# Optimization experiments

Hardware: AMD Instinct MI355X
Metric: run time of the kernel (lower is better)

Reference implementation:

```python
import jax
import jax.numpy as jnp
import numpy as np

SAMPLE_RATE = 22050
CUTOFF = 0.4 * SAMPLE_RATE  # 0.8 * (sample_rate * 0.5)
Q = 0.707  # torchaudio default


def _biquad_coeffs():
    # torchaudio.functional.lowpass_biquad coefficient formulas
    w0 = 2.0 * np.pi * CUTOFF / SAMPLE_RATE  # = 0.8*pi
    alpha = np.sin(w0) / (2.0 * Q)
    cosw = np.cos(w0)
    a0 = 1.0 + alpha
    b0 = (1.0 - cosw) / 2.0 / a0
    b1 = (1.0 - cosw) / a0
    b2 = b0
    a1 = -2.0 * cosw / a0
    a2 = (1.0 - alpha) / a0
    return np.float32(b0), np.float32(b1), np.float32(b2), np.float32(a1), np.float32(a2)


def setup_inputs() -> dict:
    key = jax.random.key(0)
    inputs = jax.random.normal(key, (64, 262144), dtype=jnp.float32)
    return {"inputs": inputs}


def reference(inputs):
    b0, b1, b2, a1, a2 = _biquad_coeffs()
    x = inputs  # [B, T]
    # FIR (numerator) part, fully parallel
    x1 = jnp.pad(x[:, :-1], ((0, 0), (1, 0)))
    x2 = jnp.pad(x[:, :-2], ((0, 0), (2, 0)))
    u = b0 * x + b1 * x1 + b2 * x2  # [B, T]

    # IIR (denominator) recurrence: y[t] = u[t] - a1*y[t-1] - a2*y[t-2]
    def step(carry, ut):
        y1, y2 = carry
        y = ut - a1 * y1 - a2 * y2
        return (y, y1), y

    z = jnp.zeros(x.shape[0], dtype=x.dtype)
    _, ys = jax.lax.scan(step, (z, z), u.T)  # scan over time, carry [B]
    # torchaudio lfilter clamps output to [-1, 1] by default
    return jnp.clip(ys.T, -1.0, 1.0)
```

## Files before the change

### kernel.cpp

```cpp
#include <hip/hip_runtime.h>
#include <math.h>

constexpr int T_LEN = 262144;
constexpr int CH    = 16;
constexpr int WARM  = 24;
constexpr int TPB   = 256;
constexpr int SEG   = TPB * CH;
constexpr int BPR   = T_LEN / SEG;
constexpr int NLD   = (CH + WARM) / 4;

__device__ __forceinline__ int sw(int i) { return i ^ (((i >> 4) & 7) << 2); }

__global__ __launch_bounds__(TPB, 6) void lowpass_kernel(
    const float* __restrict__ x, float* __restrict__ out,
    float b0, float b1, float b2, float a1, float a2)
{
    __shared__ float lds[SEG];
    const int tid = threadIdx.x;
    const size_t rbase = (size_t)(blockIdx.x / BPR) * T_LEN;
    const int seg0 = (blockIdx.x % BPR) * SEG;
    const float* __restrict__ xr = x   + rbase;
    float*       __restrict__ yr = out + rbase;

    const int w0 = seg0 + 16 * tid - WARM;
    float4 xv[NLD];
    #pragma unroll
    for (int j = 0; j < NLD; ++j) {
        const int gp = w0 + 4 * j;
        xv[j] = (gp >= 0) ? *reinterpret_cast<const float4*>(xr + gp)
                          : make_float4(0.f, 0.f, 0.f, 0.f);
    }

    float x1 = 0.f, x2 = 0.f, y1 = 0.f, y2 = 0.f;
    auto step = [&](float xc) -> float {
        const float u = fmaf(b0, xc, fmaf(b1, x1, b2 * x2));
        const float y = fmaf(-a1, y1, fmaf(-a2, y2, u));
        x2 = x1; x1 = xc; y2 = y1; y1 = y;
        return y;
    };

    #pragma unroll
    for (int j = 0; j < WARM / 4; ++j) {
        step(xv[j].x); step(xv[j].y); step(xv[j].z); step(xv[j].w);
    }
    float4 ov[CH / 4];
    #pragma unroll
    for (int k = 0; k < CH / 4; ++k) {
        const float4 v = xv[WARM / 4 + k];
        ov[k].x = fminf(fmaxf(step(v.x), -1.f), 1.f);
        ov[k].y = fminf(fmaxf(step(v.y), -1.f), 1.f);
        ov[k].z = fminf(fmaxf(step(v.z), -1.f), 1.f);
        ov[k].w = fminf(fmaxf(step(v.w), -1.f), 1.f);
    }

    #pragma unroll
    for (int k = 0; k < CH / 4; ++k)
        *reinterpret_cast<float4*>(&lds[sw(16 * tid + 4 * k)]) = ov[k];
    __syncthreads();

    #pragma unroll
    for (int j = 0; j < SEG / 4 / TPB; ++j) {
        const int m = tid + j * TPB;
        const float4 v = *reinterpret_cast<const float4*>(&lds[sw(4 * m)]);
        *reinterpret_cast<float4*>(yr + seg0 + 4 * m) = v;
    }
}

extern "C" void kernel_launch(void* const* d_in, const int* in_sizes, int n_in,
                              void* d_out, int out_size, void* d_ws, size_t ws_size,
                              hipStream_t stream) {
    const float* x = (const float*)d_in[0];
    float* out = (float*)d_out;
    const int rows = in_sizes[0] / T_LEN;

    const double SR = 22050.0, CUT = 0.4 * SR, Q = 0.707;
    double w0 = 2.0 * M_PI * CUT / SR;
    double alpha = sin(w0) / (2.0 * Q);
    double cosw = cos(w0);
    double a0d = 1.0 + alpha;
    float b0 = (float)((1.0 - cosw) / 2.0 / a0d);
    float b1 = (float)((1.0 - cosw) / a0d);
    float b2 = b0;
    float a1 = (float)(-2.0 * cosw / a0d);
    float a2 = (float)((1.0 - alpha) / a0d);

    const int blocks = rows * BPR;
    lowpass_kernel<<<blocks, TPB, 0, stream>>>(x, out, b0, b1, b2, a1, a2);
}
```

Measured before the change: 27.82 us.

## Use persistent grid with register double-buffered prefetch and nontemporal memory ops

```diff
diff --git a/kernel.cpp b/kernel.cpp
--- a/kernel.cpp
+++ b/kernel.cpp
@@ -7,62 +7,83 @@
 constexpr int TPB   = 256;
 constexpr int SEG   = TPB * CH;
 constexpr int BPR   = T_LEN / SEG;
+constexpr int ROWS  = 64;
+constexpr int NSEG  = ROWS * BPR;
+constexpr int GRID  = 1024;
+constexpr int ITERS = NSEG / GRID;
 constexpr int NLD   = (CH + WARM) / 4;
+
+typedef float f32x4 __attribute__((ext_vector_type(4)));
 
 __device__ __forceinline__ int sw(int i) { return i ^ (((i >> 4) & 7) << 2); }
 
-__global__ __launch_bounds__(TPB, 6) void lowpass_kernel(
+__global__ __launch_bounds__(TPB, 4) void lowpass_kernel(
     const float* __restrict__ x, float* __restrict__ out,
     float b0, float b1, float b2, float a1, float a2)
 {
-    __shared__ float lds[SEG];
+    __shared__ float lds[2][SEG];
     const int tid = threadIdx.x;
-    const size_t rbase = (size_t)(blockIdx.x / BPR) * T_LEN;
-    const int seg0 = (blockIdx.x % BPR) * SEG;
-    const float* __restrict__ xr = x   + rbase;
-    float*       __restrict__ yr = out + rbase;
 
-    const int w0 = seg0 + 16 * tid - WARM;
-    float4 xv[NLD];
-    #pragma unroll
-    for (int j = 0; j < NLD; ++j) {
-        const int gp = w0 + 4 * j;
-        xv[j] = (gp >= 0) ? *reinterpret_cast<const float4*>(xr + gp)
-                          : make_float4(0.f, 0.f, 0.f, 0.f);
-    }
+    f32x4 X[2][NLD];
 
-    float x1 = 0.f, x2 = 0.f, y1 = 0.f, y2 = 0.f;
-    auto step = [&](float xc) -> float {
-        const float u = fmaf(b0, xc, fmaf(b1, x1, b2 * x2));
-        const float y = fmaf(-a1, y1, fmaf(-a2, y2, u));
-        x2 = x1; x1 = xc; y2 = y1; y1 = y;
-        return y;
+    auto loadSeg = [&](int seg, f32x4 (&R)[NLD]) {
+        const int row = seg >> 6;
+        const int col = seg & (BPR - 1);
+        const float* __restrict__ xr = x + (size_t)row * T_LEN;
+        const int w0 = col * SEG + 16 * tid - WARM;
+        #pragma unroll
+        for (int j = 0; j < NLD; ++j) {
+            const int gp = w0 + 4 * j;
+            R[j] = (gp >= 0)
+                ? __builtin_nontemporal_load(
+                      reinterpret_cast<const f32x4*>(xr + gp))
+                : (f32x4)(0.f);
+        }
     };
 
+    auto processSeg = [&](int seg, const f32x4 (&R)[NLD], int buf) {
+        float x1 = 0.f, x2 = 0.f, y1 = 0.f, y2 = 0.f;
+        auto step = [&](float xc) -> float {
+            const float u = fmaf(b0, xc, fmaf(b1, x1, b2 * x2));
+            const float y = fmaf(-a1, y1, fmaf(-a2, y2, u));
+            x2 = x1; x1 = xc; y2 = y1; y1 = y;
+            return y;
+        };
+        #pragma unroll
+        for (int j = 0; j < WARM / 4; ++j) {
+            step(R[j].x); step(R[j].y); step(R[j].z); step(R[j].w);
+        }
+        f32x4 ov[CH / 4];
+        #pragma unroll
+        for (int k = 0; k < CH / 4; ++k) {
+            const f32x4 v = R[WARM / 4 + k];
+            ov[k].x = fminf(fmaxf(step(v.x), -1.f), 1.f);
+            ov[k].y = fminf(fmaxf(step(v.y), -1.f), 1.f);
+            ov[k].z = fminf(fmaxf(step(v.z), -1.f), 1.f);
+            ov[k].w = fminf(fmaxf(step(v.w), -1.f), 1.f);
+        }
+        float* L = lds[buf];
+        #pragma unroll
+        for (int k = 0; k < CH / 4; ++k)
+            *reinterpret_cast<f32x4*>(&L[sw(16 * tid + 4 * k)]) = ov[k];
+        __syncthreads();
+        const int row = seg >> 6;
+        const int col = seg & (BPR - 1);
+        float* __restrict__ yr = out + (size_t)row * T_LEN + col * SEG;
+        #pragma unroll
+        for (int j = 0; j < SEG / 4 / TPB; ++j) {
+            const int m = tid + j * TPB;
+            const f32x4 v = *reinterpret_cast<const f32x4*>(&L[sw(4 * m)]);
+            __builtin_nontemporal_store(v, reinterpret_cast<f32x4*>(yr + 4 * m));
+        }
+    };
+
+    const int s0 = blockIdx.x;
+    loadSeg(s0, X[0]);
     #pragma unroll
-    for (int j = 0; j < WARM / 4; ++j) {
-        step(xv[j].x); step(xv[j].y); step(xv[j].z); step(xv[j].w);
-    }
-    float4 ov[CH / 4];
-    #pragma unroll
-    for (int k = 0; k < CH / 4; ++k) {
-        const float4 v = xv[WARM / 4 + k];
-        ov[k].x = fminf(fmaxf(step(v.x), -1.f), 1.f);
-        ov[k].y = fminf(fmaxf(step(v.y), -1.f), 1.f);
-        ov[k].z = fminf(fmaxf(step(v.z), -1.f), 1.f);
-        ov[k].w = fminf(fmaxf(step(v.w), -1.f), 1.f);
-    }
-
-    #pragma unroll
-    for (int k = 0; k < CH / 4; ++k)
-        *reinterpret_cast<float4*>(&lds[sw(16 * tid + 4 * k)]) = ov[k];
-    __syncthreads();
-
-    #pragma unroll
-    for (int j = 0; j < SEG / 4 / TPB; ++j) {
-        const int m = tid + j * TPB;
-        const float4 v = *reinterpret_cast<const float4*>(&lds[sw(4 * m)]);
-        *reinterpret_cast<float4*>(yr + seg0 + 4 * m) = v;
+    for (int k = 0; k < ITERS; ++k) {
+        if (k + 1 < ITERS) loadSeg(s0 + (k + 1) * GRID, X[(k + 1) & 1]);
+        processSeg(s0 + k * GRID, X[k & 1], k & 1);
     }
 }
 
@@ -71,7 +92,6 @@
                               hipStream_t stream) {
     const float* x = (const float*)d_in[0];
     float* out = (float*)d_out;
-    const int rows = in_sizes[0] / T_LEN;
 
     const double SR = 22050.0, CUT = 0.4 * SR, Q = 0.707;
     double w0 = 2.0 * M_PI * CUT / SR;
@@ -84,6 +104,5 @@
     float a1 = (float)(-2.0 * cosw / a0d);
     float a2 = (float)((1.0 - alpha) / a0d);
 
-    const int blocks = rows * BPR;
-    lowpass_kernel<<<blocks, TPB, 0, stream>>>(x, out, b0, b1, b2, a1, a2);
+    lowpass_kernel<<<GRID, TPB, 0, stream>>>(x, out, b0, b1, b2, a1, a2);
 }
```

New measurement: 53.99 us. +94.1%, slower.

## Make kernel persistent with double-buffered register prefetch across four segments

Applied to the files above, without the earlier changes.

```diff
diff --git a/kernel.cpp b/kernel.cpp
--- a/kernel.cpp
+++ b/kernel.cpp
@@ -7,63 +7,89 @@
 constexpr int TPB   = 256;
 constexpr int SEG   = TPB * CH;
 constexpr int BPR   = T_LEN / SEG;
+constexpr int ROWS  = 64;
+constexpr int NSEG  = ROWS * BPR;
+constexpr int GRID  = 1024;
 constexpr int NLD   = (CH + WARM) / 4;
+
+typedef float f32x4 __attribute__((ext_vector_type(4)));
 
 __device__ __forceinline__ int sw(int i) { return i ^ (((i >> 4) & 7) << 2); }
 
-__global__ __launch_bounds__(TPB, 6) void lowpass_kernel(
+#define STEP(xc, yv)                                              \
+    {                                                             \
+        const float u_ = fmaf(b0, (xc), fmaf(b1, x1_, b2 * x2_)); \
+        (yv) = fmaf(-a1, y1_, fmaf(-a2, y2_, u_));                \
+        x2_ = x1_; x1_ = (xc); y2_ = y1_; y1_ = (yv);             \
+    }
+
+#define LOAD_SEG(R, sgc)                                                    \
+    {                                                                       \
+        const int seg_ = (sgc);                                             \
+        const int row_ = seg_ >> 6;                          \
+        const int col_ = seg_ & (BPR - 1);                                  \
+        const float* __restrict__ xr_ = x + (size_t)row_ * T_LEN;           \
+        const int w0_ = col_ * SEG + 16 * tid - WARM;      \
+        _Pragma("unroll")                                                   \
+        for (int j = 0; j < NLD; ++j) {                                     \
+            const int gp_ = w0_ + 4 * j;                                    \
+            R[j] = (gp_ >= 0) ? *reinterpret_cast<const f32x4*>(xr_ + gp_)  \
+                              : (f32x4)(0.f);                               \
+        }                                                                   \
+    }
+
+#define PROC_SEG(R, sgc, B)                                                 \
+    {                                                                       \
+        const int seg_ = (sgc);                                             \
+        float x1_ = 0.f, x2_ = 0.f, y1_ = 0.f, y2_ = 0.f, yy_;              \
+        f32x4 ov_[CH / 4];                                                  \
+        _Pragma("unroll")                                                   \
+        for (int j = 0; j < WARM / 4; ++j) {         \
+            const f32x4 v_ = R[j];                                          \
+            STEP(v_.x, yy_); STEP(v_.y, yy_);                               \
+            STEP(v_.z, yy_); STEP(v_.w, yy_);                               \
+        }                                                                   \
+        _Pragma("unroll")                                                   \
+        for (int k = 0; k < CH / 4; ++k) {            \
+            const f32x4 v_ = R[WARM / 4 + k];                               \
+            STEP(v_.x, yy_); ov_[k].x = fminf(fmaxf(yy_, -1.f), 1.f);       \
+            STEP(v_.y, yy_); ov_[k].y = fminf(fmaxf(yy_, -1.f), 1.f);       \
+            STEP(v_.z, yy_); ov_[k].z = fminf(fmaxf(yy_, -1.f), 1.f);       \
+            STEP(v_.w, yy_); ov_[k].w = fminf(fmaxf(yy_, -1.f), 1.f);       \
+        }                                                                   \
+        float* L_ = lds[B];                                                 \
+        _Pragma("unroll")                                                   \
+        for (int k = 0; k < CH / 4; ++k)                                    \
+            *reinterpret_cast<f32x4*>(&L_[sw(16 * tid + 4 * k)]) = ov_[k];  \
+        __syncthreads();                                                    \
+        const int row_ = seg_ >> 6;                                         \
+        const int col_ = seg_ & (BPR - 1);                                  \
+        float* __restrict__ yr_ = out + (size_t)row_ * T_LEN + col_ * SEG;  \
+        _Pragma("unroll")                                                   \
+        for (int j = 0; j < SEG / 4 / TPB; ++j) {      \
+            const int m_ = tid + j * TPB;                                   \
+            const f32x4 v_ =                                                \
+                *reinterpret_cast<const f32x4*>(&L_[sw(4 * m_)]);           \
+            __builtin_nontemporal_store(                                    \
+                v_, reinterpret_cast<f32x4*>(yr_ + 4 * m_));                \
+        }                                                                   \
+    }
+
+__global__ __launch_bounds__(TPB, 4) void lowpass_kernel(
     const float* __restrict__ x, float* __restrict__ out,
     float b0, float b1, float b2, float a1, float a2)
 {
-    __shared__ float lds[SEG];
+    __shared__ float lds[2][SEG];
     const int tid = threadIdx.x;
-    const size_t rbase = (size_t)(blockIdx.x / BPR) * T_LEN;
-    const int seg0 = (blockIdx.x % BPR) * SEG;
-    const float* __restrict__ xr = x   + rbase;
-    float*       __restrict__ yr = out + rbase;
+    const int s0  = blockIdx.x;
 
-    const int w0 = seg0 + 16 * tid - WARM;
-    float4 xv[NLD];
-    #pragma unroll
-    for (int j = 0; j < NLD; ++j) {
-        const int gp = w0 + 4 * j;
-        xv[j] = (gp >= 0) ? *reinterpret_cast<const float4*>(xr + gp)
-                          : make_float4(0.f, 0.f, 0.f, 0.f);
-    }
+    f32x4 XA[NLD], XB[NLD];
 
-    float x1 = 0.f, x2 = 0.f, y1 = 0.f, y2 = 0.f;
-    auto step = [&](float xc) -> float {
-        const float u = fmaf(b0, xc, fmaf(b1, x1, b2 * x2));
-        const float y = fmaf(-a1, y1, fmaf(-a2, y2, u));
-        x2 = x1; x1 = xc; y2 = y1; y1 = y;
-        return y;
-    };
-
-    #pragma unroll
-    for (int j = 0; j < WARM / 4; ++j) {
-        step(xv[j].x); step(xv[j].y); step(xv[j].z); step(xv[j].w);
-    }
-    float4 ov[CH / 4];
-    #pragma unroll
-    for (int k = 0; k < CH / 4; ++k) {
-        const float4 v = xv[WARM / 4 + k];
-        ov[k].x = fminf(fmaxf(step(v.x), -1.f), 1.f);
-        ov[k].y = fminf(fmaxf(step(v.y), -1.f), 1.f);
-        ov[k].z = fminf(fmaxf(step(v.z), -1.f), 1.f);
-        ov[k].w = fminf(fmaxf(step(v.w), -1.f), 1.f);
-    }
-
-    #pragma unroll
-    for (int k = 0; k < CH / 4; ++k)
-        *reinterpret_cast<float4*>(&lds[sw(16 * tid + 4 * k)]) = ov[k];
-    __syncthreads();
-
-    #pragma unroll
-    for (int j = 0; j < SEG / 4 / TPB; ++j) {
-        const int m = tid + j * TPB;
-        const float4 v = *reinterpret_cast<const float4*>(&lds[sw(4 * m)]);
-        *reinterpret_cast<float4*>(yr + seg0 + 4 * m) = v;
-    }
+    LOAD_SEG(XA, s0);
+    LOAD_SEG(XB, s0 + GRID);     PROC_SEG(XA, s0,            0);
+    LOAD_SEG(XA, s0 + 2 * GRID); PROC_SEG(XB, s0 + GRID,     1);
+    LOAD_SEG(XB, s0 + 3 * GRID); PROC_SEG(XA, s0 + 2 * GRID, 0);
+    PROC_SEG(XB, s0 + 3 * GRID, 1);
 }
 
 extern "C" void kernel_launch(void* const* d_in, const int* in_sizes, int n_in,
@@ -71,7 +97,6 @@
                               hipStream_t stream) {
     const float* x = (const float*)d_in[0];
     float* out = (float*)d_out;
-    const int rows = in_sizes[0] / T_LEN;
 
     const double SR = 22050.0, CUT = 0.4 * SR, Q = 0.707;
     double w0 = 2.0 * M_PI * CUT / SR;
@@ -84,6 +109,5 @@
     float a1 = (float)(-2.0 * cosw / a0d);
     float a2 = (float)((1.0 - alpha) / a0d);
 
-    const int blocks = rows * BPR;
-    lowpass_kernel<<<blocks, TPB, 0, stream>>>(x, out, b0, b1, b2, a1, a2);
+    lowpass_kernel<<<GRID, TPB, 0, stream>>>(x, out, b0, b1, b2, a1, a2);
 }
```

Result: slower. 28.78 us (+3.5%).
